# Kernel tuning notes

Measured on AMD Instinct MI355X. Metric: run time of the kernel, lower is better.

Reference implementation:

```python
import jax, jax.numpy as jnp
import numpy as np

NB_OBJECTS = 3
DIM_BODY = 10
DIM_OBJECT = 15
DIM_ACT = 4
DIM_NODE = 128
D_PHI_IN = DIM_ACT + DIM_BODY + DIM_OBJECT + DIM_NODE  # 157
HID = 256
D_PHI_OUT = 3 * D_PHI_IN  # 471
D_RHO_OUT = 1
BATCH = 65536


def _linear_init(key, fan_in, fan_out):
    # torch nn.Linear default: U(-1/sqrt(fan_in), 1/sqrt(fan_in))
    bound = 1.0 / np.sqrt(fan_in)
    k1, k2 = jax.random.split(key)
    W = jax.random.uniform(k1, (fan_in, fan_out), minval=-bound, maxval=bound, dtype=jnp.float32)
    b = jax.random.uniform(k2, (fan_out,), minval=-bound, maxval=bound, dtype=jnp.float32)
    return W, b


def setup_inputs() -> dict:
    key = jax.random.key(0)
    ks = jax.random.split(key, 11)
    obs = jax.random.normal(ks[0], (BATCH, DIM_BODY + NB_OBJECTS * DIM_OBJECT), dtype=jnp.float32)
    act = jax.random.normal(ks[1], (BATCH, DIM_ACT), dtype=jnp.float32)
    nodes = jax.random.normal(ks[2], (NB_OBJECTS, BATCH, DIM_NODE), dtype=jnp.float32)
    phi1_w1, phi1_b1 = _linear_init(ks[3], D_PHI_IN, HID)
    phi1_w2, phi1_b2 = _linear_init(ks[4], HID, D_PHI_OUT)
    phi2_w1, phi2_b1 = _linear_init(ks[5], D_PHI_IN, HID)
    phi2_w2, phi2_b2 = _linear_init(ks[6], HID, D_PHI_OUT)
    rho1_w1, rho1_b1 = _linear_init(ks[7], D_PHI_OUT, HID)
    rho1_w2, rho1_b2 = _linear_init(ks[8], HID, D_RHO_OUT)
    rho2_w1, rho2_b1 = _linear_init(ks[9], D_PHI_OUT, HID)
    rho2_w2, rho2_b2 = _linear_init(ks[10], HID, D_RHO_OUT)
    return {
        "obs": obs, "act": act, "nodes": nodes,
        "phi1_w1": phi1_w1, "phi1_b1": phi1_b1, "phi1_w2": phi1_w2, "phi1_b2": phi1_b2,
        "phi2_w1": phi2_w1, "phi2_b1": phi2_b1, "phi2_w2": phi2_w2, "phi2_b2": phi2_b2,
        "rho1_w1": rho1_w1, "rho1_b1": rho1_b1, "rho1_w2": rho1_w2, "rho1_b2": rho1_b2,
        "rho2_w1": rho2_w1, "rho2_b1": rho2_b1, "rho2_w2": rho2_w2, "rho2_b2": rho2_b2,
    }


def reference(obs, act, nodes,
              phi1_w1, phi1_b1, phi1_w2, phi1_b2,
              phi2_w1, phi2_b1, phi2_w2, phi2_b2,
              rho1_w1, rho1_b1, rho1_w2, rho1_b2,
              rho2_w1, rho2_b1, rho2_w2, rho2_b2):
    B = obs.shape[0]
    obs_body = obs[:, :DIM_BODY]                                   # [B, 10]
    # per-object slices -> [nb_objects, B, dim_object]
    obs_obj = obs[:, DIM_BODY:].reshape(B, NB_OBJECTS, DIM_OBJECT).transpose(1, 0, 2)
    shared = jnp.concatenate([act, obs_body], axis=-1)             # [B, 14]
    shared = jnp.broadcast_to(shared[None], (NB_OBJECTS, B, shared.shape[-1]))
    inp_phi = jnp.concatenate([shared, obs_obj, nodes], axis=-1)   # [3, B, 157]

    def mlp2(x, w1, b1, w2, b2):
        h = jax.nn.relu(x @ w1 + b1)
        return jax.nn.relu(h @ w2 + b2)

    # DeepSet: per-entity phi then sum over entities
    out1 = mlp2(inp_phi, phi1_w1, phi1_b1, phi1_w2, phi1_b2).sum(axis=0)  # [B, 471]
    out2 = mlp2(inp_phi, phi2_w1, phi2_b1, phi2_w2, phi2_b2).sum(axis=0)
    q1 = jax.nn.relu(out1 @ rho1_w1 + rho1_b1) @ rho1_w2 + rho1_b2        # [B, 1]
    q2 = jax.nn.relu(out2 @ rho2_w1 + rho2_b1) @ rho2_w2 + rho2_b2
    return (q1, q2)
```

## Files before the change

kernel.cpp:

```cpp
#include <hip/hip_runtime.h>
#include <hip/hip_fp16.h>

typedef _Float16 half8 __attribute__((ext_vector_type(8)));
typedef float f32x4 __attribute__((ext_vector_type(4)));

#define BATCH 65536
#define M1 196608
#define K1 192

#define GLL16(g, l) __builtin_amdgcn_global_load_lds( \
    (const __attribute__((address_space(1))) unsigned int*)(const void*)(g), \
    (__attribute__((address_space(3))) unsigned int*)(void*)(l), 16, 0, 0)

#define WAIT_VM(N) asm volatile("s_waitcnt vmcnt(" #N ")" ::: "memory")
#define SBAR() do { __builtin_amdgcn_s_barrier(); __builtin_amdgcn_sched_barrier(0); } while (0)

__global__ void prep_kernel(const float* __restrict__ p1w1, const float* __restrict__ p2w1,
                            const float* __restrict__ p1w2, const float* __restrict__ p2w2,
                            const float* __restrict__ r1w1, const float* __restrict__ r2w1,
                            const float* __restrict__ p1b1, const float* __restrict__ p2b1,
                            const float* __restrict__ p1b2, const float* __restrict__ p2b2,
                            const float* __restrict__ rb1a, const float* __restrict__ rb1b,
                            _Float16* __restrict__ W1t, _Float16* __restrict__ W2t,
                            _Float16* __restrict__ R1t, float* __restrict__ b1cat,
                            float* __restrict__ b2cat, float* __restrict__ rbias) {
    int e = blockIdx.x * 256 + threadIdx.x;
    if (e < 98304) {
        int n = e / 192, c = e % 192;
        int k = (c < 128) ? (29 + c) : (c - 128);
        float v = 0.f;
        if (c < 128 || (c - 128) < 29) v = (n < 256) ? p1w1[k * 256 + n] : p2w1[k * 256 + (n - 256)];
        W1t[e] = (_Float16)v;
        return;
    }
    e -= 98304;
    if (e < 262144) {
        int net = e >> 17, rr = e & 131071;
        int n = rr >> 8, k = rr & 255;
        const float* w = net ? p2w2 : p1w2;
        W2t[(size_t)net * 131072 + rr] = (n < 471) ? (_Float16)w[k * 471 + n] : (_Float16)0.f;
        return;
    }
    e -= 262144;
    if (e < 262144) {
        int net = e >> 17, rr = e & 131071;
        int n = rr >> 9, k = rr & 511;
        const float* w = net ? r2w1 : r1w1;
        R1t[(size_t)net * 131072 + rr] = (k < 471) ? (_Float16)w[k * 256 + n] : (_Float16)0.f;
        return;
    }
    e -= 262144;
    if (e < 512) { b1cat[e] = (e < 256) ? p1b1[e] : p2b1[e - 256]; return; }
    e -= 512;
    if (e < 1024) {
        int net = e >> 9, n = e & 511;
        b2cat[e] = (n < 471) ? (net ? p2b2 : p1b2)[n] : 0.f;
        return;
    }
    e -= 1024;
    if (e < 512) {
        int net = e >> 8, n = e & 255;
        rbias[e] = (net ? rb1b : rb1a)[n];
    }
}

__global__ void build_x(const float* __restrict__ obs, const float* __restrict__ act,
                        const float* __restrict__ nodes, _Float16* __restrict__ Xh) {
    long idx = (long)blockIdx.x * 256 + threadIdx.x;
    int ch = (int)(idx % 24);
    long r = idx / 24;
    int o = (int)(r >> 16), b = (int)(r & 65535);
    half8 v;
    if (ch < 16) {
        const float* s = nodes + r * 128 + ch * 8;
#pragma unroll
        for (int j = 0; j < 8; ++j) v[j] = (_Float16)s[j];
    } else if (ch < 20) {
#pragma unroll
        for (int j = 0; j < 8; ++j) {
            int lc = ch * 8 + j - 128;
            float f = 0.f;
            if (lc < 4)       f = act[b * 4 + lc];
            else if (lc < 14) f = obs[b * 55 + (lc - 4)];
            else if (lc < 29) f = obs[b * 55 + 10 + o * 15 + (lc - 14)];
            v[j] = (_Float16)f;
        }
    } else {
#pragma unroll
        for (int j = 0; j < 8; ++j) v[j] = (_Float16)0.f;
    }
    *(half8*)(Xh + r * 192 + ch * 8) = v;
}


__global__ __launch_bounds__(512) void gemm1(const _Float16* __restrict__ Xh,
                                             const _Float16* __restrict__ W1t,
                                             const float* __restrict__ b1cat,
                                             _Float16* __restrict__ H) {
    __shared__ _Float16 As[3][8192];
    __shared__ _Float16 Bs[3][16384];
    const int tid = threadIdx.x;
    int bid = blockIdx.x;
    int w = (bid & 7) * 384 + (bid >> 3);
    const int m0 = (w >> 1) * 128, n0 = (w & 1) * 256;
    const _Float16* Ab = Xh + (long)m0 * K1;
    const _Float16* Bb = W1t + (long)n0 * K1;
    const int wid = tid >> 6, lane = tid & 63;
    const int lm = lane & 15, lq = lane >> 4;
    const int wr = (wid >> 2) * 64, wc = (wid & 3) * 64;
    const int xv = lm & 7;
    const int srow = tid >> 3, schk = tid & 7;

    auto stage = [&](int s, _Float16* dA, _Float16* dB) {
        int ko = s * 64;
#pragma unroll
        for (int g = 0; g < 2; ++g) {
            int row = srow + g * 64, q = schk ^ (row & 7);
            GLL16(Ab + (long)row * K1 + ko + q * 8, dA + g * 4096 + wid * 512);
        }
#pragma unroll
        for (int g = 0; g < 4; ++g) {
            int row = srow + g * 64, q = schk ^ (row & 7);
            GLL16(Bb + (long)row * K1 + ko + q * 8, dB + g * 4096 + wid * 512);
        }
    };

    stage(0, &As[0][0], &Bs[0][0]);
    stage(1, &As[1][0], &Bs[1][0]);

    f32x4 acc[4][4] = {};
#pragma unroll
    for (int r = 0; r < 3; ++r) {
        if (r < 2) { WAIT_VM(6); } else { WAIT_VM(0); }
        SBAR();
        if (r + 2 < 3) stage(r + 2, &As[(r + 2) % 3][0], &Bs[(r + 2) % 3][0]);
        const _Float16* ab = &As[r % 3][0];
        const _Float16* bb = &Bs[r % 3][0];
#pragma unroll
        for (int ks = 0; ks < 2; ++ks) {
            const int off = ((ks * 4 + lq) ^ xv) * 8;
            half8 a[4], b[4];
#pragma unroll
            for (int i = 0; i < 4; ++i) a[i] = *(const half8*)(ab + (wr + i * 16 + lm) * 64 + off);
#pragma unroll
            for (int j = 0; j < 4; ++j) b[j] = *(const half8*)(bb + (wc + j * 16 + lm) * 64 + off);
#pragma unroll
            for (int i = 0; i < 4; ++i)
#pragma unroll
                for (int j = 0; j < 4; ++j)
                    acc[i][j] = __builtin_amdgcn_mfma_f32_16x16x32_f16(a[i], b[j], acc[i][j], 0, 0, 0);
        }
    }
#pragma unroll
    for (int j = 0; j < 4; ++j) {
        int n = n0 + wc + j * 16 + lm;
        int net = n >> 8, ncol = n & 255;
        float bi = b1cat[n];
        _Float16* hp = H + (long)net * ((long)M1 * 256) + ncol;
#pragma unroll
        for (int i = 0; i < 4; ++i) {
            int mrow = m0 + wr + i * 16 + lq * 4;
#pragma unroll
            for (int rg = 0; rg < 4; ++rg) {
                float v = acc[i][j][rg] + bi;
                v = v > 0.f ? v : 0.f;
                hp[(long)(mrow + rg) * 256] = (_Float16)v;
            }
        }
    }
}

__global__ __launch_bounds__(512) void gemm_sum(const _Float16* __restrict__ H,
                                                const _Float16* __restrict__ W2t,
                                                const float* __restrict__ b2cat,
                                                _Float16* __restrict__ Osum) {
    __shared__ _Float16 As[3][8192];
    __shared__ _Float16 Bs[3][16384];
    const int tid = threadIdx.x;
    int bid = blockIdx.x;
    int w = (bid & 7) * 256 + (bid >> 3);
    const int ncol = w & 1, net = (w >> 1) & 1, b0 = (w >> 2) * 128;
    const int n0 = ncol * 256;
    const _Float16* Ab = H + (long)net * ((long)M1 * 256) + (long)b0 * 256;
    const _Float16* Bb = W2t + (long)net * 131072 + (long)n0 * 256;
    const float* bp = b2cat + net * 512;
    const int wid = tid >> 6, lane = tid & 63;
    const int lm = lane & 15, lq = lane >> 4;
    const int wr = (wid >> 2) * 64, wc = (wid & 3) * 64;
    const int xv = lm & 7;
    const int srow = tid >> 3, schk = tid & 7;

    float bi[4];
#pragma unroll
    for (int j = 0; j < 4; ++j) bi[j] = bp[n0 + wc + j * 16 + lm];

    auto stage = [&](int s, _Float16* dA, _Float16* dB) {
        int obj = s >> 2, ko = (s & 3) * 64;
#pragma unroll
        for (int g = 0; g < 2; ++g) {
            int row = srow + g * 64, q = schk ^ (row & 7);
            GLL16(Ab + ((long)obj * BATCH + row) * 256 + ko + q * 8, dA + g * 4096 + wid * 512);
        }
#pragma unroll
        for (int g = 0; g < 4; ++g) {
            int row = srow + g * 64, q = schk ^ (row & 7);
            GLL16(Bb + (long)row * 256 + ko + q * 8, dB + g * 4096 + wid * 512);
        }
    };

    stage(0, &As[0][0], &Bs[0][0]);
    stage(1, &As[1][0], &Bs[1][0]);

    f32x4 acc[4][4] = {};
    f32x4 sum[4][4] = {};
#pragma unroll
    for (int r = 0; r < 12; ++r) {
        if (r < 11) { WAIT_VM(6); } else { WAIT_VM(0); }
        SBAR();
        if (r + 2 < 12) stage(r + 2, &As[(r + 2) % 3][0], &Bs[(r + 2) % 3][0]);
        const _Float16* ab = &As[r % 3][0];
        const _Float16* bb = &Bs[r % 3][0];
#pragma unroll
        for (int ks = 0; ks < 2; ++ks) {
            const int off = ((ks * 4 + lq) ^ xv) * 8;
            half8 a[4], b[4];
#pragma unroll
            for (int i = 0; i < 4; ++i) a[i] = *(const half8*)(ab + (wr + i * 16 + lm) * 64 + off);
#pragma unroll
            for (int j = 0; j < 4; ++j) b[j] = *(const half8*)(bb + (wc + j * 16 + lm) * 64 + off);
#pragma unroll
            for (int i = 0; i < 4; ++i)
#pragma unroll
                for (int j = 0; j < 4; ++j)
                    acc[i][j] = __builtin_amdgcn_mfma_f32_16x16x32_f16(a[i], b[j], acc[i][j], 0, 0, 0);
        }
        if ((r & 3) == 3) {
#pragma unroll
            for (int i = 0; i < 4; ++i)
#pragma unroll
                for (int j = 0; j < 4; ++j) {
#pragma unroll
                    for (int rg = 0; rg < 4; ++rg) {
                        float v = acc[i][j][rg] + bi[j];
                        sum[i][j][rg] += (v > 0.f ? v : 0.f);
                    }
                    acc[i][j] = f32x4{0.f, 0.f, 0.f, 0.f};
                }
        }
    }
    _Float16* op = Osum + (long)net * ((long)BATCH * 512);
#pragma unroll
    for (int j = 0; j < 4; ++j) {
        int n = n0 + wc + j * 16 + lm;
#pragma unroll
        for (int i = 0; i < 4; ++i) {
            int mrow = b0 + wr + i * 16 + lq * 4;
#pragma unroll
            for (int rg = 0; rg < 4; ++rg)
                op[(long)(mrow + rg) * 512 + n] = (_Float16)sum[i][j][rg];
        }
    }
}

__global__ __launch_bounds__(512) void gemm3q(const _Float16* __restrict__ Osum,
                                              const _Float16* __restrict__ R1t,
                                              const float* __restrict__ rbias,
                                              const float* __restrict__ r1w2,
                                              const float* __restrict__ r2w2,
                                              const float* __restrict__ r1b2,
                                              const float* __restrict__ r2b2,
                                              float* __restrict__ out) {
    __shared__ _Float16 As[3][8192];
    __shared__ _Float16 Bs[3][16384];
    __shared__ float qlds[128];
    const int tid = threadIdx.x;
    int bid = blockIdx.x;
    int w = (bid & 7) * 128 + (bid >> 3);
    const int net = w & 1, b0 = (w >> 1) * 128;
    if (tid < 128) qlds[tid] = 0.f;
    const _Float16* Ab = Osum + (long)net * ((long)BATCH * 512) + (long)b0 * 512;
    const _Float16* Bb = R1t + (long)net * 131072;
    const int wid = tid >> 6, lane = tid & 63;
    const int lm = lane & 15, lq = lane >> 4;
    const int wr = (wid >> 2) * 64, wc = (wid & 3) * 64;
    const int xv = lm & 7;
    const int srow = tid >> 3, schk = tid & 7;

    auto stage = [&](int s, _Float16* dA, _Float16* dB) {
        int ko = s * 64;
#pragma unroll
        for (int g = 0; g < 2; ++g) {
            int row = srow + g * 64, q = schk ^ (row & 7);
            GLL16(Ab + (long)row * 512 + ko + q * 8, dA + g * 4096 + wid * 512);
        }
#pragma unroll
        for (int g = 0; g < 4; ++g) {
            int row = srow + g * 64, q = schk ^ (row & 7);
            GLL16(Bb + (long)row * 512 + ko + q * 8, dB + g * 4096 + wid * 512);
        }
    };

    stage(0, &As[0][0], &Bs[0][0]);
    stage(1, &As[1][0], &Bs[1][0]);

    f32x4 acc[4][4] = {};
#pragma unroll
    for (int r = 0; r < 8; ++r) {
        if (r < 7) { WAIT_VM(6); } else { WAIT_VM(0); }
        SBAR();
        if (r + 2 < 8) stage(r + 2, &As[(r + 2) % 3][0], &Bs[(r + 2) % 3][0]);
        const _Float16* ab = &As[r % 3][0];
        const _Float16* bb = &Bs[r % 3][0];
#pragma unroll
        for (int ks = 0; ks < 2; ++ks) {
            const int off = ((ks * 4 + lq) ^ xv) * 8;
            half8 a[4], b[4];
#pragma unroll
            for (int i = 0; i < 4; ++i) a[i] = *(const half8*)(ab + (wr + i * 16 + lm) * 64 + off);
#pragma unroll
            for (int j = 0; j < 4; ++j) b[j] = *(const half8*)(bb + (wc + j * 16 + lm) * 64 + off);
#pragma unroll
            for (int i = 0; i < 4; ++i)
#pragma unroll
                for (int j = 0; j < 4; ++j)
                    acc[i][j] = __builtin_amdgcn_mfma_f32_16x16x32_f16(a[i], b[j], acc[i][j], 0, 0, 0);
        }
    }
    const float* w2 = net ? r2w2 : r1w2;
    const float* rb = rbias + net * 256;
    float w2v[4], bv[4];
#pragma unroll
    for (int j = 0; j < 4; ++j) {
        int col = wc + j * 16 + lm;
        w2v[j] = w2[col];
        bv[j] = rb[col];
    }
    f32x4 qp[4] = {};
#pragma unroll
    for (int i = 0; i < 4; ++i)
#pragma unroll
        for (int j = 0; j < 4; ++j)
#pragma unroll
            for (int rg = 0; rg < 4; ++rg) {
                float v = acc[i][j][rg] + bv[j];
                v = v > 0.f ? v : 0.f;
                qp[i][rg] += v * w2v[j];
            }
#pragma unroll
    for (int d = 1; d < 16; d <<= 1)
#pragma unroll
        for (int i = 0; i < 4; ++i)
#pragma unroll
            for (int rg = 0; rg < 4; ++rg)
                qp[i][rg] += __shfl_xor(qp[i][rg], d, 64);
    if ((lane & 15) == 0) {
#pragma unroll
        for (int i = 0; i < 4; ++i)
#pragma unroll
            for (int rg = 0; rg < 4; ++rg)
                atomicAdd(&qlds[wr + i * 16 + lq * 4 + rg], qp[i][rg]);
    }
    __syncthreads();
    if (tid < 128)
        out[(long)net * BATCH + b0 + tid] = qlds[tid] + (net ? r2b2[0] : r1b2[0]);
}

extern "C" void kernel_launch(void* const* d_in, const int* in_sizes, int n_in,
                              void* d_out, int out_size, void* d_ws, size_t ws_size,
                              hipStream_t stream) {
    const float* obs  = (const float*)d_in[0];
    const float* act  = (const float*)d_in[1];
    const float* nodes= (const float*)d_in[2];
    const float* p1w1 = (const float*)d_in[3];  const float* p1b1 = (const float*)d_in[4];
    const float* p1w2 = (const float*)d_in[5];  const float* p1b2 = (const float*)d_in[6];
    const float* p2w1 = (const float*)d_in[7];  const float* p2b1 = (const float*)d_in[8];
    const float* p2w2 = (const float*)d_in[9];  const float* p2b2 = (const float*)d_in[10];
    const float* r1w1 = (const float*)d_in[11]; const float* r1b1 = (const float*)d_in[12];
    const float* r1w2 = (const float*)d_in[13]; const float* r1b2 = (const float*)d_in[14];
    const float* r2w1 = (const float*)d_in[15]; const float* r2b1 = (const float*)d_in[16];
    const float* r2w2 = (const float*)d_in[17]; const float* r2b2 = (const float*)d_in[18];

    const size_t oW1t  = 0;
    const size_t oW2t  = 196608;
    const size_t oR1t  = 720896;
    const size_t oB1   = 1245184;
    const size_t oB2   = 1247232;
    const size_t oRB   = 1251328;
    const size_t oXO   = 1253376;
    const size_t oH    = 135471104;
    const size_t need  = 336797696;
    if (ws_size < need) return;

    char* ws = (char*)d_ws;
    _Float16* W1t  = (_Float16*)(ws + oW1t);
    _Float16* W2t  = (_Float16*)(ws + oW2t);
    _Float16* R1t  = (_Float16*)(ws + oR1t);
    float*    b1cat= (float*)(ws + oB1);
    float*    b2cat= (float*)(ws + oB2);
    float*    rbias= (float*)(ws + oRB);
    _Float16* Xh   = (_Float16*)(ws + oXO);
    _Float16* Osum = (_Float16*)(ws + oXO);
    _Float16* H    = (_Float16*)(ws + oH);
    float* out = (float*)d_out;

    prep_kernel<<<2440, 256, 0, stream>>>(p1w1, p2w1, p1w2, p2w2, r1w1, r2w1,
                                          p1b1, p2b1, p1b2, p2b2, r1b1, r2b1,
                                          W1t, W2t, R1t, b1cat, b2cat, rbias);
    build_x<<<18432, 256, 0, stream>>>(obs, act, nodes, Xh);
    gemm1<<<3072, 512, 0, stream>>>(Xh, W1t, b1cat, H);
    gemm_sum<<<2048, 512, 0, stream>>>(H, W2t, b2cat, Osum);
    gemm3q<<<1024, 512, 0, stream>>>(Osum, R1t, rbias, r1w2, r2w2, r1b2, r2b2, out);
}
```

Before: 346.8 us.

## Switch GEMMs to double-buffered 32-wide K stages with smaller tiles

```diff
diff --git a/kernel.cpp b/kernel.cpp
--- a/kernel.cpp
+++ b/kernel.cpp
@@ -11,9 +11,6 @@
 #define GLL16(g, l) __builtin_amdgcn_global_load_lds( \
     (const __attribute__((address_space(1))) unsigned int*)(const void*)(g), \
     (__attribute__((address_space(3))) unsigned int*)(void*)(l), 16, 0, 0)
-
-#define WAIT_VM(N) asm volatile("s_waitcnt vmcnt(" #N ")" ::: "memory")
-#define SBAR() do { __builtin_amdgcn_s_barrier(); __builtin_amdgcn_sched_barrier(0); } while (0)
 
 __global__ void prep_kernel(const float* __restrict__ p1w1, const float* __restrict__ p2w1,
                             const float* __restrict__ p1w2, const float* __restrict__ p2w2,
@@ -93,63 +90,56 @@
 }
 
 
-__global__ __launch_bounds__(512) void gemm1(const _Float16* __restrict__ Xh,
+__global__ __launch_bounds__(256) void gemm1(const _Float16* __restrict__ Xh,
                                              const _Float16* __restrict__ W1t,
                                              const float* __restrict__ b1cat,
                                              _Float16* __restrict__ H) {
-    __shared__ _Float16 As[3][8192];
-    __shared__ _Float16 Bs[3][16384];
+    __shared__ _Float16 As[2][4096];
+    __shared__ _Float16 Bs[2][4096];
     const int tid = threadIdx.x;
     int bid = blockIdx.x;
-    int w = (bid & 7) * 384 + (bid >> 3);
-    const int m0 = (w >> 1) * 128, n0 = (w & 1) * 256;
+    int w = (bid & 7) * 768 + (bid >> 3);
+    const int m0 = (w >> 2) * 128, n0 = (w & 3) * 128;
     const _Float16* Ab = Xh + (long)m0 * K1;
     const _Float16* Bb = W1t + (long)n0 * K1;
     const int wid = tid >> 6, lane = tid & 63;
     const int lm = lane & 15, lq = lane >> 4;
-    const int wr = (wid >> 2) * 64, wc = (wid & 3) * 64;
-    const int xv = lm & 7;
-    const int srow = tid >> 3, schk = tid & 7;
-
-    auto stage = [&](int s, _Float16* dA, _Float16* dB) {
-        int ko = s * 64;
+    const int wr = (wid >> 1) * 64, wc = (wid & 1) * 64;
+    const int srow = tid >> 2, schk = tid & 3;
+
+    auto stage = [&](int s, int buf) {
+        int ko = s * 32;
 #pragma unroll
         for (int g = 0; g < 2; ++g) {
-            int row = srow + g * 64, q = schk ^ (row & 7);
-            GLL16(Ab + (long)row * K1 + ko + q * 8, dA + g * 4096 + wid * 512);
-        }
-#pragma unroll
-        for (int g = 0; g < 4; ++g) {
-            int row = srow + g * 64, q = schk ^ (row & 7);
-            GLL16(Bb + (long)row * K1 + ko + q * 8, dB + g * 4096 + wid * 512);
+            int row = srow + g * 64, q = schk ^ ((row >> 1) & 3);
+            GLL16(Ab + (long)row * K1 + ko + q * 8, &As[buf][0] + g * 2048 + wid * 512);
+            GLL16(Bb + (long)row * K1 + ko + q * 8, &Bs[buf][0] + g * 2048 + wid * 512);
         }
     };
 
-    stage(0, &As[0][0], &Bs[0][0]);
-    stage(1, &As[1][0], &Bs[1][0]);
-
+    stage(0, 0);
+    __syncthreads();
+
+    const int cc = (lq ^ ((lm >> 1) & 3)) * 8;
     f32x4 acc[4][4] = {};
-#pragma unroll
-    for (int r = 0; r < 3; ++r) {
-        if (r < 2) { WAIT_VM(6); } else { WAIT_VM(0); }
-        SBAR();
-        if (r + 2 < 3) stage(r + 2, &As[(r + 2) % 3][0], &Bs[(r + 2) % 3][0]);
-        const _Float16* ab = &As[r % 3][0];
-        const _Float16* bb = &Bs[r % 3][0];
-#pragma unroll
-        for (int ks = 0; ks < 2; ++ks) {
-            const int off = ((ks * 4 + lq) ^ xv) * 8;
-            half8 a[4], b[4];
-#pragma unroll
-            for (int i = 0; i < 4; ++i) a[i] = *(const half8*)(ab + (wr + i * 16 + lm) * 64 + off);
-#pragma unroll
-            for (int j = 0; j < 4; ++j) b[j] = *(const half8*)(bb + (wc + j * 16 + lm) * 64 + off);
-#pragma unroll
-            for (int i = 0; i < 4; ++i)
-#pragma unroll
-                for (int j = 0; j < 4; ++j)
-                    acc[i][j] = __builtin_amdgcn_mfma_f32_16x16x32_f16(a[i], b[j], acc[i][j], 0, 0, 0);
-        }
+    int cur = 0;
+#pragma unroll
+    for (int r = 0; r < 6; ++r) {
+        if (r < 5) stage(r + 1, cur ^ 1);
+        const _Float16* ab = &As[cur][0];
+        const _Float16* bb = &Bs[cur][0];
+        half8 a[4], b[4];
+#pragma unroll
+        for (int i = 0; i < 4; ++i) a[i] = *(const half8*)(ab + (wr + i * 16 + lm) * 32 + cc);
+#pragma unroll
+        for (int j = 0; j < 4; ++j) b[j] = *(const half8*)(bb + (wc + j * 16 + lm) * 32 + cc);
+#pragma unroll
+        for (int i = 0; i < 4; ++i)
+#pragma unroll
+            for (int j = 0; j < 4; ++j)
+                acc[i][j] = __builtin_amdgcn_mfma_f32_16x16x32_f16(a[i], b[j], acc[i][j], 0, 0, 0);
+        __syncthreads();
+        cur ^= 1;
     }
 #pragma unroll
     for (int j = 0; j < 4; ++j) {
@@ -170,71 +160,60 @@
     }
 }
 
-__global__ __launch_bounds__(512) void gemm_sum(const _Float16* __restrict__ H,
+__global__ __launch_bounds__(256) void gemm_sum(const _Float16* __restrict__ H,
                                                 const _Float16* __restrict__ W2t,
                                                 const float* __restrict__ b2cat,
                                                 _Float16* __restrict__ Osum) {
-    __shared__ _Float16 As[3][8192];
-    __shared__ _Float16 Bs[3][16384];
+    __shared__ _Float16 As[2][4096];
+    __shared__ _Float16 Bs[2][4096];
     const int tid = threadIdx.x;
     int bid = blockIdx.x;
-    int w = (bid & 7) * 256 + (bid >> 3);
-    const int ncol = w & 1, net = (w >> 1) & 1, b0 = (w >> 2) * 128;
-    const int n0 = ncol * 256;
+    int w = (bid & 7) * 512 + (bid >> 3);
+    const int n0 = (w & 3) * 128, net = (w >> 2) & 1, b0 = (w >> 3) * 128;
     const _Float16* Ab = H + (long)net * ((long)M1 * 256) + (long)b0 * 256;
     const _Float16* Bb = W2t + (long)net * 131072 + (long)n0 * 256;
     const float* bp = b2cat + net * 512;
     const int wid = tid >> 6, lane = tid & 63;
     const int lm = lane & 15, lq = lane >> 4;
-    const int wr = (wid >> 2) * 64, wc = (wid & 3) * 64;
-    const int xv = lm & 7;
-    const int srow = tid >> 3, schk = tid & 7;
+    const int wr = (wid >> 1) * 64, wc = (wid & 1) * 64;
+    const int srow = tid >> 2, schk = tid & 3;
 
     float bi[4];
 #pragma unroll
     for (int j = 0; j < 4; ++j) bi[j] = bp[n0 + wc + j * 16 + lm];
 
-    auto stage = [&](int s, _Float16* dA, _Float16* dB) {
-        int obj = s >> 2, ko = (s & 3) * 64;
+    auto stage = [&](int s, int buf) {
+        int obj = s >> 3, ko = (s & 7) * 32;
 #pragma unroll
         for (int g = 0; g < 2; ++g) {
-            int row = srow + g * 64, q = schk ^ (row & 7);
-            GLL16(Ab + ((long)obj * BATCH + row) * 256 + ko + q * 8, dA + g * 4096 + wid * 512);
-        }
-#pragma unroll
-        for (int g = 0; g < 4; ++g) {
-            int row = srow + g * 64, q = schk ^ (row & 7);
-            GLL16(Bb + (long)row * 256 + ko + q * 8, dB + g * 4096 + wid * 512);
+            int row = srow + g * 64, q = schk ^ ((row >> 1) & 3);
+            GLL16(Ab + ((long)obj * BATCH + row) * 256 + ko + q * 8, &As[buf][0] + g * 2048 + wid * 512);
+            GLL16(Bb + (long)row * 256 + ko + q * 8, &Bs[buf][0] + g * 2048 + wid * 512);
         }
     };
 
-    stage(0, &As[0][0], &Bs[0][0]);
-    stage(1, &As[1][0], &Bs[1][0]);
-
+    stage(0, 0);
+    __syncthreads();
+
+    const int cc = (lq ^ ((lm >> 1) & 3)) * 8;
     f32x4 acc[4][4] = {};
     f32x4 sum[4][4] = {};
-#pragma unroll
-    for (int r = 0; r < 12; ++r) {
-        if (r < 11) { WAIT_VM(6); } else { WAIT_VM(0); }
-        SBAR();
-        if (r + 2 < 12) stage(r + 2, &As[(r + 2) % 3][0], &Bs[(r + 2) % 3][0]);
-        const _Float16* ab = &As[r % 3][0];
-        const _Float16* bb = &Bs[r % 3][0];
-#pragma unroll
-        for (int ks = 0; ks < 2; ++ks) {
-            const int off = ((ks * 4 + lq) ^ xv) * 8;
-            half8 a[4], b[4];
-#pragma unroll
-            for (int i = 0; i < 4; ++i) a[i] = *(const half8*)(ab + (wr + i * 16 + lm) * 64 + off);
-#pragma unroll
-            for (int j = 0; j < 4; ++j) b[j] = *(const half8*)(bb + (wc + j * 16 + lm) * 64 + off);
-#pragma unroll
-            for (int i = 0; i < 4; ++i)
-#pragma unroll
-                for (int j = 0; j < 4; ++j)
-                    acc[i][j] = __builtin_amdgcn_mfma_f32_16x16x32_f16(a[i], b[j], acc[i][j], 0, 0, 0);
-        }
-        if ((r & 3) == 3) {
+    int cur = 0;
+    for (int r = 0; r < 24; ++r) {
+        if (r < 23) stage(r + 1, cur ^ 1);
+        const _Float16* ab = &As[cur][0];
+        const _Float16* bb = &Bs[cur][0];
+        half8 a[4], b[4];
+#pragma unroll
+        for (int i = 0; i < 4; ++i) a[i] = *(const half8*)(ab + (wr + i * 16 + lm) * 32 + cc);
+#pragma unroll
+        for (int j = 0; j < 4; ++j) b[j] = *(const half8*)(bb + (wc + j * 16 + lm) * 32 + cc);
+#pragma unroll
+        for (int i = 0; i < 4; ++i)
+#pragma unroll
+            for (int j = 0; j < 4; ++j)
+                acc[i][j] = __builtin_amdgcn_mfma_f32_16x16x32_f16(a[i], b[j], acc[i][j], 0, 0, 0);
+        if ((r & 7) == 7) {
 #pragma unroll
             for (int i = 0; i < 4; ++i)
 #pragma unroll
@@ -247,6 +226,8 @@
                     acc[i][j] = f32x4{0.f, 0.f, 0.f, 0.f};
                 }
         }
+        __syncthreads();
+        cur ^= 1;
     }
     _Float16* op = Osum + (long)net * ((long)BATCH * 512);
 #pragma unroll
@@ -270,8 +251,8 @@
                                               const float* __restrict__ r1b2,
                                               const float* __restrict__ r2b2,
                                               float* __restrict__ out) {
-    __shared__ _Float16 As[3][8192];
-    __shared__ _Float16 Bs[3][16384];
+    __shared__ _Float16 As[2][4096];
+    __shared__ _Float16 Bs[2][8192];
     __shared__ float qlds[128];
     const int tid = threadIdx.x;
     int bid = blockIdx.x;
@@ -283,48 +264,43 @@
     const int wid = tid >> 6, lane = tid & 63;
     const int lm = lane & 15, lq = lane >> 4;
     const int wr = (wid >> 2) * 64, wc = (wid & 3) * 64;
-    const int xv = lm & 7;
-    const int srow = tid >> 3, schk = tid & 7;
-
-    auto stage = [&](int s, _Float16* dA, _Float16* dB) {
-        int ko = s * 64;
+    const int srow = tid >> 2, schk = tid & 3;
+
+    auto stage = [&](int s, int buf) {
+        int ko = s * 32;
+        {
+            int row = srow, q = schk ^ ((row >> 1) & 3);
+            GLL16(Ab + (long)row * 512 + ko + q * 8, &As[buf][0] + wid * 512);
+        }
 #pragma unroll
         for (int g = 0; g < 2; ++g) {
-            int row = srow + g * 64, q = schk ^ (row & 7);
-            GLL16(Ab + (long)row * 512 + ko + q * 8, dA + g * 4096 + wid * 512);
-        }
-#pragma unroll
-        for (int g = 0; g < 4; ++g) {
-            int row = srow + g * 64, q = schk ^ (row & 7);
-            GLL16(Bb + (long)row * 512 + ko + q * 8, dB + g * 4096 + wid * 512);
+            int row = srow + g * 128, q = schk ^ ((row >> 1) & 3);
+            GLL16(Bb + (long)row * 512 + ko + q * 8, &Bs[buf][0] + g * 4096 + wid * 512);
         }
     };
 
-    stage(0, &As[0][0], &Bs[0][0]);
-    stage(1, &As[1][0], &Bs[1][0]);
-
+    stage(0, 0);
+    __syncthreads();
+
+    const int cc = (lq ^ ((lm >> 1) & 3)) * 8;
     f32x4 acc[4][4] = {};
-#pragma unroll
-    for (int r = 0; r < 8; ++r) {
-        if (r < 7) { WAIT_VM(6); } else { WAIT_VM(0); }
-        SBAR();
-        if (r + 2 < 8) stage(r + 2, &As[(r + 2) % 3][0], &Bs[(r + 2) % 3][0]);
-        const _Float16* ab = &As[r % 3][0];
-        const _Float16* bb = &Bs[r % 3][0];
-#pragma unroll
-        for (int ks = 0; ks < 2; ++ks) {
-            const int off = ((ks * 4 + lq) ^ xv) * 8;
-            half8 a[4], b[4];
-#pragma unroll
-            for (int i = 0; i < 4; ++i) a[i] = *(const half8*)(ab + (wr + i * 16 + lm) * 64 + off);
-#pragma unroll
-            for (int j = 0; j < 4; ++j) b[j] = *(const half8*)(bb + (wc + j * 16 + lm) * 64 + off);
-#pragma unroll
-            for (int i = 0; i < 4; ++i)
-#pragma unroll
-                for (int j = 0; j < 4; ++j)
-                    acc[i][j] = __builtin_amdgcn_mfma_f32_16x16x32_f16(a[i], b[j], acc[i][j], 0, 0, 0);
-        }
+    int cur = 0;
+    for (int r = 0; r < 16; ++r) {
+        if (r < 15) stage(r + 1, cur ^ 1);
+        const _Float16* ab = &As[cur][0];
+        const _Float16* bb = &Bs[cur][0];
+        half8 a[4], b[4];
+#pragma unroll
+        for (int i = 0; i < 4; ++i) a[i] = *(const half8*)(ab + (wr + i * 16 + lm) * 32 + cc);
+#pragma unroll
+        for (int j = 0; j < 4; ++j) b[j] = *(const half8*)(bb + (wc + j * 16 + lm) * 32 + cc);
+#pragma unroll
+        for (int i = 0; i < 4; ++i)
+#pragma unroll
+            for (int j = 0; j < 4; ++j)
+                acc[i][j] = __builtin_amdgcn_mfma_f32_16x16x32_f16(a[i], b[j], acc[i][j], 0, 0, 0);
+        __syncthreads();
+        cur ^= 1;
     }
     const float* w2 = net ? r2w2 : r1w2;
     const float* rb = rbias + net * 256;
@@ -407,7 +383,7 @@
                                           p1b1, p2b1, p1b2, p2b2, r1b1, r2b1,
                                           W1t, W2t, R1t, b1cat, b2cat, rbias);
     build_x<<<18432, 256, 0, stream>>>(obs, act, nodes, Xh);
-    gemm1<<<3072, 512, 0, stream>>>(Xh, W1t, b1cat, H);
-    gemm_sum<<<2048, 512, 0, stream>>>(H, W2t, b2cat, Osum);
+    gemm1<<<6144, 256, 0, stream>>>(Xh, W1t, b1cat, H);
+    gemm_sum<<<4096, 256, 0, stream>>>(H, W2t, b2cat, Osum);
     gemm3q<<<1024, 512, 0, stream>>>(Osum, R1t, rbias, r1w2, r2w2, r1b2, r2b2, out);
 }
```

Result: slower. 391.5 us (+12.9%).
